# Optimization experiments

Hardware: AMD Instinct MI355X
Metric: run time of the kernel (lower is better)

Reference implementation:

```python
import jax, jax.numpy as jnp
import numpy as np

B, D, N, H = 8, 256, 2048, 4  # batch, d_model, seq_len, heads
HEAD_DIM = D // H


def _proj(x, W, b):
    # Conv1D(kernel_size=1) applied to (b, n, d) == dense over channels.
    # x: (B, D, N); W: (D, D) [in, out]; b: (D,) -> (B, D, N)
    return jnp.einsum('bdn,do->bon', x, W) + b[None, :, None]


def setup_inputs() -> dict:
    key = jax.random.key(0)
    ks = jax.random.split(key, 11)
    s = 0.02
    inp = {
        'query': jax.random.normal(ks[0], (B, D, N), jnp.float32),
        'key':   jax.random.normal(ks[1], (B, D, N), jnp.float32),
        'value': jax.random.normal(ks[2], (B, D, N), jnp.float32),
        'Wq': jax.random.normal(ks[3], (D, D), jnp.float32) * s,
        'bq': jnp.zeros((D,), jnp.float32),
        'Wk': jax.random.normal(ks[4], (D, D), jnp.float32) * s,
        'bk': jnp.zeros((D,), jnp.float32),
        'Wv': jax.random.normal(ks[5], (D, D), jnp.float32) * s,
        'bv': jnp.zeros((D,), jnp.float32),
        'Wm': jax.random.normal(ks[6], (D, D), jnp.float32) * s,
        'bm': jnp.zeros((D,), jnp.float32),
    }
    return inp


def reference(query, key, value, Wq, bq, Wk, bk, Wv, bv, Wm, bm):
    b = query.shape[0]
    # project and split heads: (B, D, N) -> (B, head_dim, H, N)
    # NOTE: TF reshape splits d_model as (head_dim, heads) with head_dim outer.
    q = _proj(query, Wq, bq).reshape(b, HEAD_DIM, H, N)
    k = _proj(key,   Wk, bk).reshape(b, HEAD_DIM, H, N)
    v = _proj(value, Wv, bv).reshape(b, HEAD_DIM, H, N)
    # attention with scale 1/sqrt(head_dim)
    scores = jnp.einsum('bdhn,bdhm->bhnm', q, k) / jnp.sqrt(jnp.asarray(HEAD_DIM, q.dtype))
    prob = jax.nn.softmax(scores, axis=-1)
    x = jnp.einsum('bhnm,bdhm->bdhn', prob, v)  # (B, head_dim, H, N)
    x = x.reshape(b, D, N)
    return _proj(x, Wm, bm)
```

## Files before the change

kernel.cpp:

```cpp
#include <hip/hip_runtime.h>
#include <stdint.h>

#define BB 8
#define DD 256
#define NN 2048
#define HH 4
#define HD 64
#define SCALE_Q 0.18033688011112042f

typedef __attribute__((ext_vector_type(8))) short bf16x8;
typedef __attribute__((ext_vector_type(4))) float f32x4;
typedef __attribute__((ext_vector_type(16))) float f32x16;


__device__ __forceinline__ void gld16(const void* g, void* l) {
  __builtin_amdgcn_global_load_lds(
      (__attribute__((address_space(1))) void*)(void*)(uintptr_t)(g),
      (__attribute__((address_space(3))) void*)(l), 16, 0, 0);
}

__device__ __forceinline__ unsigned short f2bf(float f) {
  union { float f; unsigned u; } v; v.f = f;
  unsigned lsb = (v.u >> 16) & 1u;
  v.u += 0x7fffu + lsb;
  return (unsigned short)(v.u >> 16);
}


__global__ __launch_bounds__(256) void tcast_x(
    const float* __restrict__ q, const float* __restrict__ k,
    const float* __restrict__ v, unsigned short* __restrict__ oq,
    unsigned short* __restrict__ ok2, unsigned short* __restrict__ ov) {
  __shared__ float t[64][65];
  int z = blockIdx.z, src = z >> 3, b = z & 7;
  const float* ip = (src == 0 ? q : src == 1 ? k : v) + (long)b * DD * NN;
  unsigned short* op = (src == 0 ? oq : src == 1 ? ok2 : ov) + (long)b * NN * DD;
  int c0 = blockIdx.x * 64, r0 = blockIdx.y * 64;
  int tx = threadIdx.x & 63, ty = threadIdx.x >> 6;
#pragma unroll
  for (int rr = 0; rr < 16; rr++) {
    int r = rr * 4 + ty;
    t[r][tx] = ip[(long)(r0 + r) * NN + c0 + tx];
  }
  __syncthreads();
#pragma unroll
  for (int rr = 0; rr < 16; rr++) {
    int c = rr * 4 + ty;
    op[(long)(c0 + c) * DD + r0 + tx] = f2bf(t[tx][c]);
  }
}


__global__ __launch_bounds__(256) void tcast_w(
    const float* __restrict__ Wq, const float* __restrict__ Wk,
    const float* __restrict__ Wv, const float* __restrict__ Wm,
    unsigned short* __restrict__ oWq, unsigned short* __restrict__ oWk,
    unsigned short* __restrict__ oWv, unsigned short* __restrict__ oWm) {
  __shared__ float t[32][33];
  int z = blockIdx.z;
  const float* ip = z == 0 ? Wq : z == 1 ? Wk : z == 2 ? Wv : Wm;
  unsigned short* op = z == 0 ? oWq : z == 1 ? oWk : z == 2 ? oWv : oWm;
  float s = z == 0 ? SCALE_Q : 1.f;
  int c0 = blockIdx.x * 32, r0 = blockIdx.y * 32;
  int tx = threadIdx.x & 31, ty = threadIdx.x >> 5;
#pragma unroll
  for (int rr = 0; rr < 4; rr++) {
    int r = rr * 8 + ty;
    t[r][tx] = ip[(long)(r0 + r) * DD + c0 + tx];
  }
  __syncthreads();
  if (z < 3) {
#pragma unroll
    for (int rr = 0; rr < 4; rr++) {
      int c = rr * 8 + ty;
      int o = c0 + c;
      int jp = ((o & 3) << 6) | (o >> 2);
      op[(long)jp * DD + r0 + tx] = f2bf(s * t[tx][c]);
    }
  } else {
#pragma unroll
    for (int rr = 0; rr < 4; rr++) {
      int c = rr * 8 + ty;
      int d = r0 + tx;
      int kp = ((d & 3) << 6) | (d >> 2);
      op[(long)(c0 + c) * DD + kp] = f2bf(t[tx][c]);
    }
  }
}


#define GEMM_STAGE(kt, buf)                                                    \
  {                                                                            \
    int _kt = (kt);                                                            \
    _Pragma("unroll") for (int c = 0; c < 4; c++) {                            \
      int row = w * 32 + c * 8 + (lane >> 3);                                  \
      int so = ((lane & 7) * 16) ^ ((row & 7) << 4);                           \
      gld16((const char*)Ag + ((long)(i0 + row) * DD + _kt * 64) * 2 + so,     \
            (char*)&At[buf][0] + (w * 32 + c * 8) * 128);                      \
    }                                                                          \
    _Pragma("unroll") for (int c = 0; c < 2; c++) {                            \
      int row = w * 16 + c * 8 + (lane >> 3);                                  \
      int so = ((lane & 7) * 16) ^ ((row & 7) << 4);                           \
      gld16((const char*)Bg + ((long)(j0 + row) * DD + _kt * 64) * 2 + so,     \
            (char*)&Bt[buf][0] + (w * 16 + c * 8) * 128);                      \
    }                                                                          \
  }

#define GEMM_COMPUTE(buf)                                                      \
  _Pragma("unroll") for (int ks = 0; ks < 2; ks++) {                           \
    bf16x8 af[4], bfv[2];                                                      \
    _Pragma("unroll") for (int mi = 0; mi < 4; mi++) {                         \
      int row = wr * 64 + mi * 16 + (lane & 15);                               \
      int off = (ks * 64 + (lane >> 4) * 16) ^ ((row & 7) << 4);               \
      af[mi] = *(const bf16x8*)((const char*)&At[buf][0] + row * 128 + off);   \
    }                                                                          \
    _Pragma("unroll") for (int nj = 0; nj < 2; nj++) {                         \
      int row = wc * 32 + nj * 16 + (lane & 15);                               \
      int off = (ks * 64 + (lane >> 4) * 16) ^ ((row & 7) << 4);               \
      bfv[nj] = *(const bf16x8*)((const char*)&Bt[buf][0] + row * 128 + off);  \
    }                                                                          \
    _Pragma("unroll") for (int mi = 0; mi < 4; mi++)                           \
        _Pragma("unroll") for (int nj = 0; nj < 2; nj++)                       \
            acc[mi][nj] = __builtin_amdgcn_mfma_f32_16x16x32_bf16(             \
                af[mi], bfv[nj], acc[mi][nj], 0, 0, 0);                        \
  }

#define GEMM_MAIN()                                                            \
  f32x4 acc[4][2];                                                             \
  _Pragma("unroll") for (int a = 0; a < 4; a++)                                \
      _Pragma("unroll") for (int c = 0; c < 2; c++)                            \
          acc[a][c] = (f32x4){0.f, 0.f, 0.f, 0.f};                             \
  GEMM_STAGE(0, 0);                                                            \
  __syncthreads();                                                             \
  int buf = 0;                                                                 \
  for (int kt = 0; kt < 4; kt++) {                                             \
    if (kt < 3) GEMM_STAGE(kt + 1, buf ^ 1);                                   \
    GEMM_COMPUTE(buf);                                                         \
    __syncthreads();                                                           \
    buf ^= 1;                                                                  \
  }


__global__ __launch_bounds__(256) void gemm_qkv(
    const unsigned short* __restrict__ Xq, const unsigned short* __restrict__ Xk,
    const unsigned short* __restrict__ Xv, const unsigned short* __restrict__ Wq,
    const unsigned short* __restrict__ Wk, const unsigned short* __restrict__ Wv,
    const float* __restrict__ bq, const float* __restrict__ bk,
    const float* __restrict__ bv, unsigned short* __restrict__ Qh,
    unsigned short* __restrict__ Kh, unsigned short* __restrict__ Vh) {
  __shared__ unsigned short At[2][128 * 64], Bt[2][64 * 64];
  int z = blockIdx.z, proj = z >> 3, bb = z & 7;
  int flat = blockIdx.y * 16 + blockIdx.x;
  const unsigned short *Ag, *Bg;
  const float* bias;
  float bsc = 1.f;
  int i0, j0;
  if (proj == 0) {
    Ag = Xq + (long)bb * NN * DD; Bg = Wq; bias = bq; bsc = SCALE_Q;
    i0 = (flat & 15) * 128; j0 = (flat >> 4) * 64;
  } else if (proj == 1) {
    Ag = Xk + (long)bb * NN * DD; Bg = Wk; bias = bk;
    i0 = (flat & 15) * 128; j0 = (flat >> 4) * 64;
  } else {
    Ag = Wv; Bg = Xv + (long)bb * NN * DD; bias = bv;
    i0 = (flat >> 5) * 128; j0 = (flat & 31) * 64;
  }
  int tid = threadIdx.x, lane = tid & 63, w = tid >> 6;
  int wr = w >> 1, wc = w & 1;

  GEMM_MAIN();

#pragma unroll
  for (int mi = 0; mi < 4; mi++) {
#pragma unroll
    for (int nj = 0; nj < 2; nj++) {
#pragma unroll
      for (int r = 0; r < 4; r++) {
        int ig = i0 + wr * 64 + mi * 16 + (lane >> 4) * 4 + r;
        int jg = j0 + wc * 32 + nj * 16 + (lane & 15);
        float v = acc[mi][nj][r];
        if (proj < 2) {
          int o = ((jg & 63) << 2) | (jg >> 6);
          v += bias[o] * bsc;
          int hh = jg >> 6, hd = jg & 63;
          unsigned short* dst = proj == 0 ? Qh : Kh;
          dst[(((long)bb * HH + hh) * NN + ig) * HD + hd] = f2bf(v);
        } else {
          int o = ((ig & 63) << 2) | (ig >> 6);
          v += bias[o];
          int hh = ig >> 6, hd = ig & 63;
          Vh[(((long)bb * HH + hh) * HD + hd) * NN + jg] = f2bf(v);
        }
      }
    }
  }
}


__global__ __launch_bounds__(256) void gemm_out(
    const unsigned short* __restrict__ A, const unsigned short* __restrict__ B,
    const float* __restrict__ bias, float* __restrict__ out) {
  __shared__ unsigned short At[2][128 * 64], Bt[2][64 * 64];
  int bb = blockIdx.z;
  int flat = blockIdx.y * 16 + blockIdx.x;
  const unsigned short* Ag = A;
  const unsigned short* Bg = B + (long)bb * NN * DD;
  int i0 = (flat >> 5) * 128, j0 = (flat & 31) * 64;
  int tid = threadIdx.x, lane = tid & 63, w = tid >> 6;
  int wr = w >> 1, wc = w & 1;

  GEMM_MAIN();

#pragma unroll
  for (int mi = 0; mi < 4; mi++) {
#pragma unroll
    for (int nj = 0; nj < 2; nj++) {
#pragma unroll
      for (int r = 0; r < 4; r++) {
        int ig = i0 + wr * 64 + mi * 16 + (lane >> 4) * 4 + r;
        int jg = j0 + wc * 32 + nj * 16 + (lane & 15);
        out[((long)bb * DD + ig) * NN + jg] = acc[mi][nj][r] + bias[ig];
      }
    }
  }
}


__global__ __launch_bounds__(256) void attn_kernel(
    const unsigned short* __restrict__ Q, const unsigned short* __restrict__ Kg,
    const unsigned short* __restrict__ V, unsigned short* __restrict__ XA) {
  __shared__ unsigned short Vt[2][64 * 64];
  int h = blockIdx.y, b = blockIdx.z;
  int tid = threadIdx.x, lane = tid & 63, w = tid >> 6;
  int l31 = lane & 31, hi = lane >> 5;
  int q0 = blockIdx.x * 128 + w * 32;
  long hb = (long)b * HH + h;
  const unsigned short* Qb = Q + hb * NN * HD;
  const unsigned short* Kb = Kg + hb * NN * HD;
  const unsigned short* Vb = V + hb * HD * NN;

  bf16x8 qf[4];
#pragma unroll
  for (int ks = 0; ks < 4; ks++)
    qf[ks] = *(const bf16x8*)(Qb + (long)(q0 + l31) * HD + ks * 16 + hi * 8);

  f32x16 oA[2];
#pragma unroll
  for (int hf = 0; hf < 2; hf++)
#pragma unroll
    for (int r = 0; r < 16; r++) oA[hf][r] = 0.f;
  float lsum = 0.f;

  auto stageV = [&](int vbuf, int t) {
    int m0 = t * 64;
#pragma unroll
    for (int c = 0; c < 2; c++) {
      int row = w * 16 + c * 8 + (lane >> 3);
      int so = ((lane & 7) * 16) ^ ((row & 7) << 4);
      gld16((const char*)Vb + ((long)row * NN + m0) * 2 + so,
            (char*)&Vt[vbuf][0] + (w * 16 + c * 8) * 128);
    }
  };
  auto loadK = [&](bf16x8 (&kf)[8], int t) {
    int m0 = t * 64;
#pragma unroll
    for (int kh = 0; kh < 2; kh++)
#pragma unroll
      for (int ks = 0; ks < 4; ks++)
        kf[kh * 4 + ks] =
            *(const bf16x8*)(Kb + (long)(m0 + kh * 32 + l31) * HD + ks * 16 + hi * 8);
  };
  auto body = [&](const bf16x8 (&kf)[8], int vbuf) {
#pragma unroll
    for (int kh = 0; kh < 2; kh++) {
      f32x16 s;
#pragma unroll
      for (int r = 0; r < 16; r++) s[r] = 0.f;
      __builtin_amdgcn_s_setprio(1);
#pragma unroll
      for (int ks = 0; ks < 4; ks++)
        s = __builtin_amdgcn_mfma_f32_32x32x16_bf16(kf[kh * 4 + ks], qf[ks], s, 0, 0, 0);
      __builtin_amdgcn_s_setprio(0);
      float p[16];
#pragma unroll
      for (int r = 0; r < 16; r++) {
        p[r] = __builtin_amdgcn_exp2f(s[r]);
        lsum += p[r];
      }
      unsigned pk[8];
#pragma unroll
      for (int i = 0; i < 8; i++)
        asm("v_cvt_pk_bf16_f32 %0, %1, %2"
            : "=v"(pk[i]) : "v"(p[2 * i]), "v"(p[2 * i + 1]));
      asm volatile("v_permlane32_swap_b32 %0, %1" : "+v"(pk[0]), "+v"(pk[2]));
      asm volatile("v_permlane32_swap_b32 %0, %1" : "+v"(pk[1]), "+v"(pk[3]));
      asm volatile("v_permlane32_swap_b32 %0, %1" : "+v"(pk[4]), "+v"(pk[6]));
      asm volatile("v_permlane32_swap_b32 %0, %1" : "+v"(pk[5]), "+v"(pk[7]));
#pragma unroll
      for (int sv = 0; sv < 2; sv++) {
        union { bf16x8 v; unsigned u[4]; } fr;
        fr.u[0] = pk[sv * 4 + 0]; fr.u[1] = pk[sv * 4 + 1];
        fr.u[2] = pk[sv * 4 + 2]; fr.u[3] = pk[sv * 4 + 3];
        __builtin_amdgcn_s_setprio(1);
#pragma unroll
        for (int hf = 0; hf < 2; hf++) {
          int vrow = hf * 32 + l31;
          int voff = ((2 * kh + sv) * 32 + hi * 16) ^ ((vrow & 7) << 4);
          bf16x8 vf = *(const bf16x8*)((const char*)&Vt[vbuf][0] + vrow * 128 + voff);
          oA[hf] = __builtin_amdgcn_mfma_f32_32x32x16_bf16(fr.v, vf, oA[hf], 0, 0, 0);
        }
        __builtin_amdgcn_s_setprio(0);
      }
    }
  };

  bf16x8 kfA[8], kfB[8];
  loadK(kfA, 0);
  stageV(0, 0);
  __syncthreads();

  for (int t = 0; t < NN / 64; t += 2) {
    stageV(1, t + 1);
    loadK(kfB, t + 1);
    body(kfA, 0);
    __syncthreads();
    if (t + 2 < NN / 64) {
      stageV(0, t + 2);
      loadK(kfA, t + 2);
    }
    body(kfB, 1);
    __syncthreads();
  }

  float lt = lsum + __shfl_xor(lsum, 32);
#pragma unroll
  for (int r = 0; r < 16; r++) {
    int qrow = (r & 3) + 8 * (r >> 2) + 4 * hi;
    float linv = 1.0f / __shfl(lt, qrow);
    long nrow = (long)b * NN + q0 + qrow;
#pragma unroll
    for (int hf = 0; hf < 2; hf++) {
      float val = oA[hf][r] * linv;
      XA[nrow * DD + h * HD + hf * 32 + l31] = f2bf(val);
    }
  }
}


extern "C" void kernel_launch(void* const* d_in, const int* in_sizes, int n_in,
                              void* d_out, int out_size, void* d_ws, size_t ws_size,
                              hipStream_t stream) {
  const float* q_in = (const float*)d_in[0];
  const float* k_in = (const float*)d_in[1];
  const float* v_in = (const float*)d_in[2];
  const float* Wq = (const float*)d_in[3];
  const float* bq = (const float*)d_in[4];
  const float* Wk = (const float*)d_in[5];
  const float* bk = (const float*)d_in[6];
  const float* Wv = (const float*)d_in[7];
  const float* bv = (const float*)d_in[8];
  const float* Wm = (const float*)d_in[9];
  const float* bm = (const float*)d_in[10];
  float* out = (float*)d_out;

  const long SX = (long)BB * NN * DD;
  const long SW = (long)DD * DD;
  unsigned short* Xqt = (unsigned short*)d_ws;
  unsigned short* Xkt = Xqt + SX;
  unsigned short* Xvt = Xkt + SX;
  unsigned short* Qh = Xvt + SX;
  unsigned short* Kh = Qh + SX;
  unsigned short* Vh = Kh + SX;
  unsigned short* Wqt = Vh + SX;
  unsigned short* Wkt = Wqt + SW;
  unsigned short* Wvt = Wkt + SW;
  unsigned short* Wmt = Wvt + SW;
  unsigned short* XAt = Xqt;
  if (ws_size < (size_t)(6 * SX + 4 * SW) * 2) return;

  dim3 blk(256);
  tcast_x<<<dim3(NN / 64, DD / 64, 24), blk, 0, stream>>>(
      q_in, k_in, v_in, Xqt, Xkt, Xvt);
  tcast_w<<<dim3(DD / 32, DD / 32, 4), blk, 0, stream>>>(
      Wq, Wk, Wv, Wm, Wqt, Wkt, Wvt, Wmt);
  gemm_qkv<<<dim3(16, 4, 24), blk, 0, stream>>>(
      Xqt, Xkt, Xvt, Wqt, Wkt, Wvt, bq, bk, bv, Qh, Kh, Vh);
  attn_kernel<<<dim3(NN / 128, HH, BB), blk, 0, stream>>>(Qh, Kh, Vh, XAt);
  gemm_out<<<dim3(16, 4, 8), blk, 0, stream>>>(Wmt, XAt, bm, out);
}
```

Baseline: 215.8 us.

## Process two query tiles per wave and stage K through LDS

Each wave now handles 64 query rows (two 32-row groups) instead of 32. The K tile is staged into shared memory with async global-to-LDS loads alongside V, so each K fragment feeds two score MFMAs and each V fragment feeds two output MFMAs. The grid drops to 256 blocks with a remapped block index that spreads (batch, head, query-block) work across the XCDs. This cuts per-wave global K traffic and raises MFMA reuse, but doubles accumulator register pressure and halves the number of blocks, which may leave CUs underfilled.

```diff
diff --git a/kernel.cpp b/kernel.cpp
--- a/kernel.cpp
+++ b/kernel.cpp
@@ -229,119 +229,140 @@
 __global__ __launch_bounds__(256) void attn_kernel(
     const unsigned short* __restrict__ Q, const unsigned short* __restrict__ Kg,
     const unsigned short* __restrict__ V, unsigned short* __restrict__ XA) {
+  __shared__ unsigned short Kt[2][64 * 64];
   __shared__ unsigned short Vt[2][64 * 64];
-  int h = blockIdx.y, b = blockIdx.z;
+  int flat = blockIdx.x;
+  int work = (flat & 7) * 32 + (flat >> 3);
+  int qb = work & 7, h = (work >> 3) & 3, b = work >> 5;
   int tid = threadIdx.x, lane = tid & 63, w = tid >> 6;
   int l31 = lane & 31, hi = lane >> 5;
-  int q0 = blockIdx.x * 128 + w * 32;
+  int qw = qb * 256 + w * 64;
   long hb = (long)b * HH + h;
   const unsigned short* Qb = Q + hb * NN * HD;
   const unsigned short* Kb = Kg + hb * NN * HD;
   const unsigned short* Vb = V + hb * HD * NN;
 
-  bf16x8 qf[4];
-#pragma unroll
-  for (int ks = 0; ks < 4; ks++)
-    qf[ks] = *(const bf16x8*)(Qb + (long)(q0 + l31) * HD + ks * 16 + hi * 8);
-
-  f32x16 oA[2];
-#pragma unroll
-  for (int hf = 0; hf < 2; hf++)
-#pragma unroll
-    for (int r = 0; r < 16; r++) oA[hf][r] = 0.f;
-  float lsum = 0.f;
-
-  auto stageV = [&](int vbuf, int t) {
+  bf16x8 qf[2][4];
+#pragma unroll
+  for (int g = 0; g < 2; g++)
+#pragma unroll
+    for (int ks = 0; ks < 4; ks++)
+      qf[g][ks] =
+          *(const bf16x8*)(Qb + (long)(qw + g * 32 + l31) * HD + ks * 16 + hi * 8);
+
+  f32x16 oA[2][2];
+#pragma unroll
+  for (int g = 0; g < 2; g++)
+#pragma unroll
+    for (int hf = 0; hf < 2; hf++)
+#pragma unroll
+      for (int r = 0; r < 16; r++) oA[g][hf][r] = 0.f;
+  float lsum0 = 0.f, lsum1 = 0.f;
+
+  auto stage = [&](int buf, int t) {
     int m0 = t * 64;
 #pragma unroll
     for (int c = 0; c < 2; c++) {
       int row = w * 16 + c * 8 + (lane >> 3);
       int so = ((lane & 7) * 16) ^ ((row & 7) << 4);
+      gld16((const char*)Kb + (long)(m0 + row) * 128 + so,
+            (char*)&Kt[buf][0] + (w * 16 + c * 8) * 128);
       gld16((const char*)Vb + ((long)row * NN + m0) * 2 + so,
-            (char*)&Vt[vbuf][0] + (w * 16 + c * 8) * 128);
+            (char*)&Vt[buf][0] + (w * 16 + c * 8) * 128);
     }
   };
-  auto loadK = [&](bf16x8 (&kf)[8], int t) {
-    int m0 = t * 64;
-#pragma unroll
-    for (int kh = 0; kh < 2; kh++)
-#pragma unroll
-      for (int ks = 0; ks < 4; ks++)
-        kf[kh * 4 + ks] =
-            *(const bf16x8*)(Kb + (long)(m0 + kh * 32 + l31) * HD + ks * 16 + hi * 8);
-  };
-  auto body = [&](const bf16x8 (&kf)[8], int vbuf) {
+
+  int cur = 0;
+  stage(0, 0);
+  __syncthreads();
+
+  for (int t = 0; t < NN / 64; t++) {
+    if (t + 1 < NN / 64) stage(cur ^ 1, t + 1);
+
 #pragma unroll
     for (int kh = 0; kh < 2; kh++) {
-      f32x16 s;
-#pragma unroll
-      for (int r = 0; r < 16; r++) s[r] = 0.f;
+      bf16x8 kf[4];
+#pragma unroll
+      for (int ks = 0; ks < 4; ks++) {
+        int row = kh * 32 + l31;
+        int off = (ks * 32 + hi * 16) ^ ((row & 7) << 4);
+        kf[ks] = *(const bf16x8*)((const char*)&Kt[cur][0] + row * 128 + off);
+      }
+      f32x16 s0, s1;
+#pragma unroll
+      for (int r = 0; r < 16; r++) { s0[r] = 0.f; s1[r] = 0.f; }
       __builtin_amdgcn_s_setprio(1);
 #pragma unroll
-      for (int ks = 0; ks < 4; ks++)
-        s = __builtin_amdgcn_mfma_f32_32x32x16_bf16(kf[kh * 4 + ks], qf[ks], s, 0, 0, 0);
+      for (int ks = 0; ks < 4; ks++) {
+        s0 = __builtin_amdgcn_mfma_f32_32x32x16_bf16(kf[ks], qf[0][ks], s0, 0, 0, 0);
+        s1 = __builtin_amdgcn_mfma_f32_32x32x16_bf16(kf[ks], qf[1][ks], s1, 0, 0, 0);
+      }
       __builtin_amdgcn_s_setprio(0);
-      float p[16];
+      unsigned pk0[8], pk1[8];
 #pragma unroll
       for (int r = 0; r < 16; r++) {
-        p[r] = __builtin_amdgcn_exp2f(s[r]);
-        lsum += p[r];
-      }
-      unsigned pk[8];
+        s0[r] = __builtin_amdgcn_exp2f(s0[r]);
+        lsum0 += s0[r];
+      }
 #pragma unroll
       for (int i = 0; i < 8; i++)
         asm("v_cvt_pk_bf16_f32 %0, %1, %2"
-            : "=v"(pk[i]) : "v"(p[2 * i]), "v"(p[2 * i + 1]));
-      asm volatile("v_permlane32_swap_b32 %0, %1" : "+v"(pk[0]), "+v"(pk[2]));
-      asm volatile("v_permlane32_swap_b32 %0, %1" : "+v"(pk[1]), "+v"(pk[3]));
-      asm volatile("v_permlane32_swap_b32 %0, %1" : "+v"(pk[4]), "+v"(pk[6]));
-      asm volatile("v_permlane32_swap_b32 %0, %1" : "+v"(pk[5]), "+v"(pk[7]));
+            : "=v"(pk0[i]) : "v"(s0[2 * i]), "v"(s0[2 * i + 1]));
+#pragma unroll
+      for (int r = 0; r < 16; r++) {
+        s1[r] = __builtin_amdgcn_exp2f(s1[r]);
+        lsum1 += s1[r];
+      }
+#pragma unroll
+      for (int i = 0; i < 8; i++)
+        asm("v_cvt_pk_bf16_f32 %0, %1, %2"
+            : "=v"(pk1[i]) : "v"(s1[2 * i]), "v"(s1[2 * i + 1]));
+      asm volatile("v_permlane32_swap_b32 %0, %1" : "+v"(pk0[0]), "+v"(pk0[2]));
+      asm volatile("v_permlane32_swap_b32 %0, %1" : "+v"(pk0[1]), "+v"(pk0[3]));
+      asm volatile("v_permlane32_swap_b32 %0, %1" : "+v"(pk0[4]), "+v"(pk0[6]));
+      asm volatile("v_permlane32_swap_b32 %0, %1" : "+v"(pk0[5]), "+v"(pk0[7]));
+      asm volatile("v_permlane32_swap_b32 %0, %1" : "+v"(pk1[0]), "+v"(pk1[2]));
+      asm volatile("v_permlane32_swap_b32 %0, %1" : "+v"(pk1[1]), "+v"(pk1[3]));
+      asm volatile("v_permlane32_swap_b32 %0, %1" : "+v"(pk1[4]), "+v"(pk1[6]));
+      asm volatile("v_permlane32_swap_b32 %0, %1" : "+v"(pk1[5]), "+v"(pk1[7]));
 #pragma unroll
       for (int sv = 0; sv < 2; sv++) {
-        union { bf16x8 v; unsigned u[4]; } fr;
-        fr.u[0] = pk[sv * 4 + 0]; fr.u[1] = pk[sv * 4 + 1];
-        fr.u[2] = pk[sv * 4 + 2]; fr.u[3] = pk[sv * 4 + 3];
+        union { bf16x8 v; unsigned u[4]; } fr0, fr1;
+#pragma unroll
+        for (int u = 0; u < 4; u++) {
+          fr0.u[u] = pk0[sv * 4 + u];
+          fr1.u[u] = pk1[sv * 4 + u];
+        }
         __builtin_amdgcn_s_setprio(1);
 #pragma unroll
         for (int hf = 0; hf < 2; hf++) {
           int vrow = hf * 32 + l31;
           int voff = ((2 * kh + sv) * 32 + hi * 16) ^ ((vrow & 7) << 4);
-          bf16x8 vf = *(const bf16x8*)((const char*)&Vt[vbuf][0] + vrow * 128 + voff);
-          oA[hf] = __builtin_amdgcn_mfma_f32_32x32x16_bf16(fr.v, vf, oA[hf], 0, 0, 0);
+          bf16x8 vf = *(const bf16x8*)((const char*)&Vt[cur][0] + vrow * 128 + voff);
+          oA[0][hf] = __builtin_amdgcn_mfma_f32_32x32x16_bf16(fr0.v, vf, oA[0][hf], 0, 0, 0);
+          oA[1][hf] = __builtin_amdgcn_mfma_f32_32x32x16_bf16(fr1.v, vf, oA[1][hf], 0, 0, 0);
         }
         __builtin_amdgcn_s_setprio(0);
       }
     }
-  };
-
-  bf16x8 kfA[8], kfB[8];
-  loadK(kfA, 0);
-  stageV(0, 0);
-  __syncthreads();
-
-  for (int t = 0; t < NN / 64; t += 2) {
-    stageV(1, t + 1);
-    loadK(kfB, t + 1);
-    body(kfA, 0);
     __syncthreads();
-    if (t + 2 < NN / 64) {
-      stageV(0, t + 2);
-      loadK(kfA, t + 2);
-    }
-    body(kfB, 1);
-    __syncthreads();
-  }
-
-  float lt = lsum + __shfl_xor(lsum, 32);
-#pragma unroll
-  for (int r = 0; r < 16; r++) {
-    int qrow = (r & 3) + 8 * (r >> 2) + 4 * hi;
-    float linv = 1.0f / __shfl(lt, qrow);
-    long nrow = (long)b * NN + q0 + qrow;
-#pragma unroll
-    for (int hf = 0; hf < 2; hf++) {
-      float val = oA[hf][r] * linv;
-      XA[nrow * DD + h * HD + hf * 32 + l31] = f2bf(val);
+    cur ^= 1;
+  }
+
+#pragma unroll
+  for (int g = 0; g < 2; g++) {
+    float ls = g == 0 ? lsum0 : lsum1;
+    float lt = ls + __shfl_xor(ls, 32);
+#pragma unroll
+    for (int r = 0; r < 16; r++) {
+      int qrow = (r & 3) + 8 * (r >> 2) + 4 * hi;
+      float linv = 1.0f / __shfl(lt, qrow);
+      long nrow = (long)b * NN + qw + g * 32 + qrow;
+#pragma unroll
+      for (int hf = 0; hf < 2; hf++) {
+        float val = oA[g][hf][r] * linv;
+        XA[nrow * DD + h * HD + hf * 32 + l31] = f2bf(val);
+      }
     }
   }
 }
@@ -385,6 +406,6 @@
       Wq, Wk, Wv, Wm, Wqt, Wkt, Wvt, Wmt);
   gemm_qkv<<<dim3(16, 4, 24), blk, 0, stream>>>(
       Xqt, Xkt, Xvt, Wqt, Wkt, Wvt, bq, bk, bv, Qh, Kh, Vh);
-  attn_kernel<<<dim3(NN / 128, HH, BB), blk, 0, stream>>>(Qh, Kh, Vh, XAt);
+  attn_kernel<<<dim3(256), blk, 0, stream>>>(Qh, Kh, Vh, XAt);
   gemm_out<<<dim3(16, 4, 8), blk, 0, stream>>>(Wmt, XAt, bm, out);
 }
```

New measurement: 203.1 us. 1.06x faster.

## Stage K tiles through LDS, remap attention blocks for XCD locality, vectorize transpose-cast

Applied to the files above, without the earlier changes.

The attention kernel now loads K tiles into a double-buffered, swizzled LDS buffer with async global-to-LDS loads, as V already was. Previously each wave read K straight from global memory into registers. The grid is flattened to 512 blocks and remapped so blocks sharing a (batch, head) land on the same XCD, which should help L2 reuse of K/V. The setprio hints and the two-tile unrolled loop are dropped, and the input transpose-cast kernel now uses float4 loads and 4-wide bf16 stores. LDS use doubles and every K fragment now goes through LDS reads, so occupancy and LDS bandwidth pressure may change.

```diff
diff --git a/kernel.cpp b/kernel.cpp
--- a/kernel.cpp
+++ b/kernel.cpp
@@ -11,6 +11,7 @@
 typedef __attribute__((ext_vector_type(8))) short bf16x8;
 typedef __attribute__((ext_vector_type(4))) float f32x4;
 typedef __attribute__((ext_vector_type(16))) float f32x16;
+typedef __attribute__((ext_vector_type(4))) unsigned short u16x4;
 
 
 __device__ __forceinline__ void gld16(const void* g, void* l) {
@@ -36,17 +37,25 @@
   const float* ip = (src == 0 ? q : src == 1 ? k : v) + (long)b * DD * NN;
   unsigned short* op = (src == 0 ? oq : src == 1 ? ok2 : ov) + (long)b * NN * DD;
   int c0 = blockIdx.x * 64, r0 = blockIdx.y * 64;
-  int tx = threadIdx.x & 63, ty = threadIdx.x >> 6;
-#pragma unroll
-  for (int rr = 0; rr < 16; rr++) {
-    int r = rr * 4 + ty;
-    t[r][tx] = ip[(long)(r0 + r) * NN + c0 + tx];
+  int id = threadIdx.x;
+  int hi4 = id >> 4, lo4 = id & 15;
+#pragma unroll
+  for (int r = 0; r < 4; r++) {
+    int d = r * 16 + hi4;
+    float4 vv = *(const float4*)(ip + (long)(r0 + d) * NN + c0 + lo4 * 4);
+    t[d][lo4 * 4 + 0] = vv.x;
+    t[d][lo4 * 4 + 1] = vv.y;
+    t[d][lo4 * 4 + 2] = vv.z;
+    t[d][lo4 * 4 + 3] = vv.w;
   }
   __syncthreads();
 #pragma unroll
-  for (int rr = 0; rr < 16; rr++) {
-    int c = rr * 4 + ty;
-    op[(long)(c0 + c) * DD + r0 + tx] = f2bf(t[tx][c]);
+  for (int rr = 0; rr < 4; rr++) {
+    int n = rr * 16 + hi4;
+    u16x4 o4;
+#pragma unroll
+    for (int j = 0; j < 4; j++) o4[j] = f2bf(t[lo4 * 4 + j][n]);
+    *(u16x4*)(op + (long)(c0 + n) * DD + r0 + lo4 * 4) = o4;
   }
 }
 
@@ -229,16 +238,23 @@
 __global__ __launch_bounds__(256) void attn_kernel(
     const unsigned short* __restrict__ Q, const unsigned short* __restrict__ Kg,
     const unsigned short* __restrict__ V, unsigned short* __restrict__ XA) {
+  __shared__ unsigned short Kt[2][64 * 64];
   __shared__ unsigned short Vt[2][64 * 64];
-  int h = blockIdx.y, b = blockIdx.z;
+  int flat = blockIdx.x;
+  int work = (flat & 7) * 64 + (flat >> 3);
+  int qb = work & 15, hbid = work >> 4;
+  int h = hbid & 3, b = hbid >> 2;
   int tid = threadIdx.x, lane = tid & 63, w = tid >> 6;
   int l31 = lane & 31, hi = lane >> 5;
-  int q0 = blockIdx.x * 128 + w * 32;
+  int q0 = qb * 128 + w * 32;
   long hb = (long)b * HH + h;
   const unsigned short* Qb = Q + hb * NN * HD;
   const unsigned short* Kb = Kg + hb * NN * HD;
   const unsigned short* Vb = V + hb * HD * NN;
 
+  const f32x16 FZ = {0.f, 0.f, 0.f, 0.f, 0.f, 0.f, 0.f, 0.f,
+                     0.f, 0.f, 0.f, 0.f, 0.f, 0.f, 0.f, 0.f};
+
   bf16x8 qf[4];
 #pragma unroll
   for (int ks = 0; ks < 4; ks++)
@@ -251,36 +267,37 @@
     for (int r = 0; r < 16; r++) oA[hf][r] = 0.f;
   float lsum = 0.f;
 
-  auto stageV = [&](int vbuf, int t) {
+  auto stage = [&](int buf, int t) {
     int m0 = t * 64;
 #pragma unroll
     for (int c = 0; c < 2; c++) {
       int row = w * 16 + c * 8 + (lane >> 3);
       int so = ((lane & 7) * 16) ^ ((row & 7) << 4);
+      gld16((const char*)Kb + (long)(m0 + row) * 128 + so,
+            (char*)&Kt[buf][0] + (w * 16 + c * 8) * 128);
       gld16((const char*)Vb + ((long)row * NN + m0) * 2 + so,
-            (char*)&Vt[vbuf][0] + (w * 16 + c * 8) * 128);
+            (char*)&Vt[buf][0] + (w * 16 + c * 8) * 128);
     }
   };
-  auto loadK = [&](bf16x8 (&kf)[8], int t) {
-    int m0 = t * 64;
-#pragma unroll
-    for (int kh = 0; kh < 2; kh++)
-#pragma unroll
-      for (int ks = 0; ks < 4; ks++)
-        kf[kh * 4 + ks] =
-            *(const bf16x8*)(Kb + (long)(m0 + kh * 32 + l31) * HD + ks * 16 + hi * 8);
-  };
-  auto body = [&](const bf16x8 (&kf)[8], int vbuf) {
+
+  int cur = 0;
+  stage(0, 0);
+  __syncthreads();
+
+  for (int t = 0; t < NN / 64; t++) {
+    if (t + 1 < NN / 64) stage(cur ^ 1, t + 1);
+
 #pragma unroll
     for (int kh = 0; kh < 2; kh++) {
       f32x16 s;
 #pragma unroll
-      for (int r = 0; r < 16; r++) s[r] = 0.f;
-      __builtin_amdgcn_s_setprio(1);
-#pragma unroll
-      for (int ks = 0; ks < 4; ks++)
-        s = __builtin_amdgcn_mfma_f32_32x32x16_bf16(kf[kh * 4 + ks], qf[ks], s, 0, 0, 0);
-      __builtin_amdgcn_s_setprio(0);
+      for (int ks = 0; ks < 4; ks++) {
+        int row = kh * 32 + l31;
+        int off = (ks * 32 + hi * 16) ^ ((row & 7) << 4);
+        bf16x8 kf = *(const bf16x8*)((const char*)&Kt[cur][0] + row * 128 + off);
+        s = __builtin_amdgcn_mfma_f32_32x32x16_bf16(kf, qf[ks],
+                                                    ks == 0 ? FZ : s, 0, 0, 0);
+      }
       float p[16];
 #pragma unroll
       for (int r = 0; r < 16; r++) {
@@ -301,35 +318,17 @@
         union { bf16x8 v; unsigned u[4]; } fr;
         fr.u[0] = pk[sv * 4 + 0]; fr.u[1] = pk[sv * 4 + 1];
         fr.u[2] = pk[sv * 4 + 2]; fr.u[3] = pk[sv * 4 + 3];
-        __builtin_amdgcn_s_setprio(1);
 #pragma unroll
         for (int hf = 0; hf < 2; hf++) {
           int vrow = hf * 32 + l31;
           int voff = ((2 * kh + sv) * 32 + hi * 16) ^ ((vrow & 7) << 4);
-          bf16x8 vf = *(const bf16x8*)((const char*)&Vt[vbuf][0] + vrow * 128 + voff);
+          bf16x8 vf = *(const bf16x8*)((const char*)&Vt[cur][0] + vrow * 128 + voff);
           oA[hf] = __builtin_amdgcn_mfma_f32_32x32x16_bf16(fr.v, vf, oA[hf], 0, 0, 0);
         }
-        __builtin_amdgcn_s_setprio(0);
-      }
-    }
-  };
-
-  bf16x8 kfA[8], kfB[8];
-  loadK(kfA, 0);
-  stageV(0, 0);
-  __syncthreads();
-
-  for (int t = 0; t < NN / 64; t += 2) {
-    stageV(1, t + 1);
-    loadK(kfB, t + 1);
-    body(kfA, 0);
+      }
+    }
     __syncthreads();
-    if (t + 2 < NN / 64) {
-      stageV(0, t + 2);
-      loadK(kfA, t + 2);
-    }
-    body(kfB, 1);
-    __syncthreads();
+    cur ^= 1;
   }
 
   float lt = lsum + __shfl_xor(lsum, 32);
@@ -385,6 +384,6 @@
       Wq, Wk, Wv, Wm, Wqt, Wkt, Wvt, Wmt);
   gemm_qkv<<<dim3(16, 4, 24), blk, 0, stream>>>(
       Xqt, Xkt, Xvt, Wqt, Wkt, Wvt, bq, bk, bv, Qh, Kh, Vh);
-  attn_kernel<<<dim3(NN / 128, HH, BB), blk, 0, stream>>>(Qh, Kh, Vh, XAt);
+  attn_kernel<<<dim3(512), blk, 0, stream>>>(Qh, Kh, Vh, XAt);
   gemm_out<<<dim3(16, 4, 8), blk, 0, stream>>>(Wmt, XAt, bm, out);
 }
```

Result: faster. 192.0 us (-11.0%).
